# Performance work log

Hardware: AMD Instinct MI355X
Metric: run time of the kernel (lower is better)

Reference implementation:

```python
import jax, jax.numpy as jnp
import numpy as np

B, T, D = 1, 2048, 4096
H, G = 32, 8
HD = D // H          # 128
REP = H // G         # 4
KV_DIM = 2 * HD * G  # 2048


def setup_inputs() -> dict:
    key = jax.random.key(0)
    k0, k1, k2, k3 = jax.random.split(key, 4)
    x = jax.random.normal(k0, (B, T, D), dtype=jnp.float32)
    Wq = jax.random.normal(k1, (D, D), dtype=jnp.float32) * 0.02
    Wkv = jax.random.normal(k2, (D, KV_DIM), dtype=jnp.float32) * 0.02
    Wo = jax.random.normal(k3, (D, D), dtype=jnp.float32) * 0.02
    bo = jnp.zeros((D,), dtype=jnp.float32)
    return {"x": x, "Wq": Wq, "Wkv": Wkv, "Wo": Wo, "bo": bo}


def reference(x, Wq, Wkv, Wo, bo):
    b, t, d = x.shape
    # projections (qkv_bias=False)
    q = jnp.dot(x, Wq).reshape(b, t, H, HD).transpose(0, 2, 1, 3)        # (b,H,t,hd)
    kv = jnp.dot(x, Wkv).reshape(b, t, G, 2, HD).transpose(2, 3, 0, 1, 4)  # (G,2,b,t,hd)
    k, v = kv[:, 0], kv[:, 1]                                             # (G,b,t,hd)
    # faithful to torch: unsqueeze+repeat then flat view(b, H, t, hd)
    k = jnp.broadcast_to(k[:, :, None], (G, b, REP, t, HD)).reshape(b, H, t, HD)
    v = jnp.broadcast_to(v[:, :, None], (G, b, REP, t, HD)).reshape(b, H, t, HD)
    # attention: mask then scale, matching original order
    scores = jnp.einsum('bhqd,bhkd->bhqk', q, k)                          # (b,H,t,t)
    causal = jnp.triu(jnp.ones((t, t), dtype=bool), 1)
    scores = jnp.where(causal[None, None], -jnp.inf, scores)
    weights = jax.nn.softmax(scores * (1.0 / HD ** 0.5), axis=-1)
    ctx = jnp.einsum('bhqk,bhkd->bhqd', weights, v)                       # (b,H,t,hd)
    ctx = ctx.transpose(0, 2, 1, 3).reshape(b, t, d)
    return jnp.dot(ctx, Wo) + bo
```

## Files before the change

### kernel.cpp

```cpp
#include <hip/hip_runtime.h>

#define T_SEQ 2048
#define D_MODEL 4096
#define NH 32
#define NG 8
#define HD 128

typedef unsigned short u16;
typedef __bf16 bf16x8 __attribute__((ext_vector_type(8)));
typedef float f32x4 __attribute__((ext_vector_type(4)));

#define AS1 __attribute__((address_space(1)))
#define AS3 __attribute__((address_space(3)))

__device__ __forceinline__ void async_cp16(const u16* g, u16* l) {
  __builtin_amdgcn_global_load_lds((AS1 void*)g, (AS3 void*)l, 16, 0, 0);
}

__device__ __forceinline__ u16 f2bf(float f){
  union { float f; unsigned x; } v; v.f = f;
  unsigned r = v.x + 0x7FFFu + ((v.x >> 16) & 1u);
  return (u16)(r >> 16);
}
__device__ __forceinline__ u16 to_bf(float f){ return f2bf(f); }
__device__ __forceinline__ u16 to_bf(u16 u){ return u; }

__global__ __launch_bounds__(256) void cvt_k(const float* __restrict__ in,
                                             u16* __restrict__ out, int n4)
{
  int i = blockIdx.x * 256 + threadIdx.x;
  if (i >= n4) return;
  float4 v = *(const float4*)&in[(size_t)i * 4];
  short4 o;
  o.x = (short)f2bf(v.x); o.y = (short)f2bf(v.y);
  o.z = (short)f2bf(v.z); o.w = (short)f2bf(v.w);
  *(short4*)&out[(size_t)i * 4] = o;
}

template<typename TIN>
__global__ __launch_bounds__(256) void transpose_k(const TIN* __restrict__ in,
                                                   u16* __restrict__ out, int R, int C)
{
  int z = blockIdx.z;
  in  += (size_t)z * R * C;
  out += (size_t)z * R * C;
  __shared__ __align__(16) u16 tile[32][36];
  int c0 = blockIdx.x * 32, r0 = blockIdx.y * 32;
  int t = threadIdx.x;
  int lr = t >> 3, lc = (t & 7) * 4;
  const TIN* src = &in[(size_t)(r0 + lr) * C + c0 + lc];
  #pragma unroll
  for (int i = 0; i < 4; i++) tile[lr][lc + i] = to_bf(src[i]);
  __syncthreads();
  short4 v;
  v.x = (short)tile[lc + 0][lr];
  v.y = (short)tile[lc + 1][lr];
  v.z = (short)tile[lc + 2][lr];
  v.w = (short)tile[lc + 3][lr];
  *(short4*)&out[(size_t)(c0 + lr) * R + r0 + lc] = v;
}

template<int MODE>
__global__ __launch_bounds__(256) void gemm_k(
    const u16* __restrict__ A, const u16* __restrict__ BT,
    u16* __restrict__ Cout, u16* __restrict__ Kout, u16* __restrict__ Vout,
    float* __restrict__ Fout, const float* __restrict__ bias, int K, int N)
{
  __shared__ __align__(16) u16 sA[128 * 64];
  __shared__ __align__(16) u16 sB[128 * 64];
  const int t = threadIdx.x;
  const int lane = t & 63, wave = t >> 6;
  const int quad = lane >> 4, lm = lane & 15;
  const int wm = wave >> 1, wn = wave & 1;
  const int m0 = blockIdx.y * 128, n0 = blockIdx.x * 128;
  const f32x4 fzero = {0.f, 0.f, 0.f, 0.f};

  const int sr_sub = lane >> 3;
  const int sgl = (lane & 7) ^ sr_sub;

  f32x4 acc[4][4];
  #pragma unroll
  for (int i = 0; i < 4; i++)
    #pragma unroll
    for (int j = 0; j < 4; j++) acc[i][j] = fzero;

  for (int k0 = 0; k0 < K; k0 += 64) {
    #pragma unroll
    for (int c = 0; c < 4; c++) {
      int r = c * 32 + wave * 8 + sr_sub;
      async_cp16(&A [(size_t)(m0 + r) * K + k0 + sgl * 8], &sA[(c * 256 + wave * 64) * 8]);
      async_cp16(&BT[(size_t)(n0 + r) * K + k0 + sgl * 8], &sB[(c * 256 + wave * 64) * 8]);
    }
    __syncthreads();
    #pragma unroll
    for (int kb = 0; kb < 2; kb++) {
      bf16x8 af[4], bfr[4];
      #pragma unroll
      for (int mt = 0; mt < 4; mt++) {
        int row = wm * 64 + mt * 16 + lm;
        af[mt] = *(const bf16x8*)&sA[row * 64 + (((kb * 4 + quad) ^ (lm & 7)) * 8)];
      }
      #pragma unroll
      for (int nt = 0; nt < 4; nt++) {
        int row = wn * 64 + nt * 16 + lm;
        bfr[nt] = *(const bf16x8*)&sB[row * 64 + (((kb * 4 + quad) ^ (lm & 7)) * 8)];
      }
      #pragma unroll
      for (int mt = 0; mt < 4; mt++)
        #pragma unroll
        for (int nt = 0; nt < 4; nt++)
          acc[mt][nt] = __builtin_amdgcn_mfma_f32_16x16x32_bf16(af[mt], bfr[nt], acc[mt][nt], 0, 0, 0);
    }
    __syncthreads();
  }

  #pragma unroll
  for (int mt = 0; mt < 4; mt++) {
    #pragma unroll
    for (int nt = 0; nt < 4; nt++) {
      #pragma unroll
      for (int r = 0; r < 4; r++) {
        int grow = m0 + wm * 64 + mt * 16 + quad * 4 + r;
        int gcol = n0 + wn * 64 + nt * 16 + lm;
        float v = acc[mt][nt][r];
        if (MODE == 0) {
          Cout[(size_t)grow * N + gcol] = f2bf(v);
        } else if (MODE == 1) {
          int g = gcol >> 8, s = (gcol >> 7) & 1, hd = gcol & 127;
          u16* dst = s ? Vout : Kout;
          dst[((size_t)g * T_SEQ + grow) * HD + hd] = f2bf(v);
        } else {
          Fout[(size_t)grow * N + gcol] = v + bias[gcol];
        }
      }
    }
  }
}

__global__ __launch_bounds__(256) void attn_k(
    const u16* __restrict__ Q, const u16* __restrict__ Kb,
    const u16* __restrict__ Vt, u16* __restrict__ ctx)
{
  __shared__ __align__(16) u16 sK[2 * 64 * 128];
  __shared__ __align__(16) u16 sV[2 * 128 * 64];
  __shared__ __align__(16) u16 sP[4 * 16 * 72];
  const int t = threadIdx.x;
  const int lane = t & 63, wave = t >> 6;
  const int quad = lane >> 4, lm = lane & 15;

  const int id = blockIdx.x + gridDim.x * blockIdx.y;
  const int g = id & 7;
  const int idx = id >> 3;
  const int h = g * 4 + (idx & 3);
  const int q0 = (31 - (idx >> 2)) * 64;
  const int nt = (q0 >> 6) + 1;

  const float scale = 0.088388347648318447f;
  const float C1 = scale * 1.4426950408889634f;
  const float C2 = -14.0f * 1.4426950408889634f;
  const f32x4 fzero = {0.f, 0.f, 0.f, 0.f};

  bf16x8 aq[4];
  {
    const u16* qp = Q + (size_t)(q0 + wave * 16 + lm) * D_MODEL + h * HD + quad * 8;
    #pragma unroll
    for (int kb = 0; kb < 4; kb++) aq[kb] = *(const bf16x8*)(qp + kb * 32);
  }
  f32x4 o[8];
  #pragma unroll
  for (int i = 0; i < 8; i++) o[i] = fzero;
  float l4[4];
  #pragma unroll
  for (int r = 0; r < 4; r++) l4[r] = 0.f;

  const u16* Kg = Kb + (size_t)g * T_SEQ * HD;
  const u16* Vg = Vt + (size_t)g * HD * T_SEQ;
  u16* sPw = sP + wave * 16 * 72;

  const int k_r_sub = lane >> 4;
  const int v_r_sub = lane >> 3;
  const int v_gl = (lane & 7) ^ v_r_sub;

  auto stage = [&](int td) {
    const int kv0 = td << 6;
    u16* dK = sK + (td & 1) * (64 * 128);
    u16* dV = sV + (td & 1) * (128 * 64);
    #pragma unroll
    for (int c = 0; c < 4; c++) {
      int rk = c * 16 + wave * 4 + k_r_sub;
      int kgl = (lane & 15) ^ (rk & 7);
      async_cp16(&Kg[(size_t)(kv0 + rk) * HD + kgl * 8], &dK[(c * 256 + wave * 64) * 8]);
      int rv = c * 32 + wave * 8 + v_r_sub;
      async_cp16(&Vg[(size_t)rv * T_SEQ + kv0 + v_gl * 8], &dV[(c * 256 + wave * 64) * 8]);
    }
  };

  stage(0);
  if (nt > 1) stage(1);

  for (int ti = 0; ti < nt; ++ti) {
    if (ti + 1 < nt) { asm volatile("s_waitcnt vmcnt(8)" ::: "memory"); }
    else             { asm volatile("s_waitcnt vmcnt(0)" ::: "memory"); }
    __builtin_amdgcn_s_barrier();

    const u16* cK = sK + (ti & 1) * (64 * 128);
    const u16* cV = sV + (ti & 1) * (128 * 64);
    const int kv0 = ti << 6;

    f32x4 s[4];
    __builtin_amdgcn_s_setprio(1);
    #pragma unroll
    for (int nt4 = 0; nt4 < 4; nt4++) {
      s[nt4] = fzero;
      #pragma unroll
      for (int kb = 0; kb < 4; kb++) {
        int row = nt4 * 16 + lm;
        bf16x8 bk = *(const bf16x8*)&cK[row * 128 + (((kb * 4 + quad) ^ (lm & 7)) * 8)];
        s[nt4] = __builtin_amdgcn_mfma_f32_16x16x32_bf16(aq[kb], bk, s[nt4], 0, 0, 0);
      }
    }
    __builtin_amdgcn_s_setprio(0);

    #pragma unroll
    for (int r = 0; r < 4; r++) {
      int qr = q0 + wave * 16 + quad * 4 + r;
      #pragma unroll
      for (int nt4 = 0; nt4 < 4; nt4++) {
        int kvc = kv0 + nt4 * 16 + lm;
        float p = exp2f(fmaf(s[nt4][r], C1, C2));
        p = (kvc > qr) ? 0.f : p;
        l4[r] += p;
        sPw[(quad * 4 + r) * 72 + nt4 * 16 + lm] = f2bf(p);
      }
    }

    __builtin_amdgcn_s_setprio(1);
    #pragma unroll
    for (int kb2 = 0; kb2 < 2; kb2++) {
      bf16x8 ap = *(const bf16x8*)&sPw[lm * 72 + kb2 * 32 + quad * 8];
      #pragma unroll
      for (int n8 = 0; n8 < 8; n8++) {
        int row = n8 * 16 + lm;
        bf16x8 bv = *(const bf16x8*)&cV[row * 64 + (((kb2 * 4 + quad) ^ (lm & 7)) * 8)];
        o[n8] = __builtin_amdgcn_mfma_f32_16x16x32_bf16(ap, bv, o[n8], 0, 0, 0);
      }
    }
    __builtin_amdgcn_s_setprio(0);

    __builtin_amdgcn_s_barrier();
    if (ti + 2 < nt) stage(ti + 2);
  }

  #pragma unroll
  for (int r = 0; r < 4; r++) {
    #pragma unroll
    for (int off = 1; off < 16; off <<= 1) l4[r] += __shfl_xor(l4[r], off, 64);
  }

  #pragma unroll
  for (int r = 0; r < 4; r++) {
    float inv = 1.f / l4[r];
    #pragma unroll
    for (int n8 = 0; n8 < 8; n8++) {
      ctx[(size_t)(q0 + wave * 16 + quad * 4 + r) * D_MODEL + h * HD + n8 * 16 + lm]
          = f2bf(o[n8][r] * inv);
    }
  }
}

extern "C" void kernel_launch(void* const* d_in, const int* in_sizes, int n_in,
                              void* d_out, int out_size, void* d_ws, size_t ws_size,
                              hipStream_t stream)
{
  const float* x   = (const float*)d_in[0];
  const float* Wq  = (const float*)d_in[1];
  const float* Wkv = (const float*)d_in[2];
  const float* Wo  = (const float*)d_in[3];
  const float* bo  = (const float*)d_in[4];
  float* out = (float*)d_out;

  char* ws = (char*)d_ws;
  const size_t SZ_T   = 33554432;
  const size_t SZ_ACT = 16777216;
  const size_t SZ_KV  = 4194304;
  u16* Tb = (u16*)(ws);
  u16* Xb = (u16*)(ws + SZ_T);
  u16* Qb = (u16*)(ws + SZ_T + SZ_ACT);
  u16* Cx = (u16*)(ws + SZ_T + 2 * SZ_ACT);
  u16* Kb = (u16*)(ws + SZ_T + 3 * SZ_ACT);
  u16* Vb = (u16*)(ws + SZ_T + 3 * SZ_ACT + SZ_KV);
  u16* Vt = (u16*)(ws + SZ_T + 3 * SZ_ACT + 2 * SZ_KV);

  cvt_k<<<dim3(8192, 1, 1), 256, 0, stream>>>(x, Xb, 2097152);
  transpose_k<float><<<dim3(128, 128, 1), 256, 0, stream>>>(Wq, Tb, 4096, 4096);
  gemm_k<0><<<dim3(32, 16, 1), 256, 0, stream>>>(Xb, Tb, Qb, nullptr, nullptr, nullptr, nullptr, 4096, 4096);
  transpose_k<float><<<dim3(64, 128, 1), 256, 0, stream>>>(Wkv, Tb, 4096, 2048);
  gemm_k<1><<<dim3(16, 16, 1), 256, 0, stream>>>(Xb, Tb, nullptr, Kb, Vb, nullptr, nullptr, 4096, 2048);
  transpose_k<u16><<<dim3(4, 64, 8), 256, 0, stream>>>(Vb, Vt, 2048, 128);
  attn_k<<<dim3(32, 32, 1), 256, 0, stream>>>(Qb, Kb, Vt, Cx);
  transpose_k<float><<<dim3(128, 128, 1), 256, 0, stream>>>(Wo, Tb, 4096, 4096);
  gemm_k<2><<<dim3(32, 16, 1), 256, 0, stream>>>(Cx, Tb, nullptr, nullptr, nullptr, out, bo, 4096, 4096);
}
```

Measured before the change: 516.2 us.

## Double-buffer GEMM LDS tiles and write V transposed from KV GEMM epilogue

The GEMM kernel now double-buffers its A/B LDS tiles, prefetching two k-steps ahead with async global-to-LDS copies, partial vmcnt waits and raw barriers, mirroring the attention kernel's pipeline. The aim is to overlap global loads with MFMA work instead of serialising load then compute. The KV-projection epilogue also writes V directly in transposed layout with packed short4 stores, removing the separate V transpose kernel and its buffer. Doubling LDS use per block may reduce occupancy, and the transposed V stores are strided across rows.

```diff
diff --git a/kernel.cpp b/kernel.cpp
--- a/kernel.cpp
+++ b/kernel.cpp
@@ -66,13 +66,14 @@
     u16* __restrict__ Cout, u16* __restrict__ Kout, u16* __restrict__ Vout,
     float* __restrict__ Fout, const float* __restrict__ bias, int K, int N)
 {
-  __shared__ __align__(16) u16 sA[128 * 64];
-  __shared__ __align__(16) u16 sB[128 * 64];
+  __shared__ __align__(16) u16 sA[2 * 128 * 64];
+  __shared__ __align__(16) u16 sB[2 * 128 * 64];
   const int t = threadIdx.x;
   const int lane = t & 63, wave = t >> 6;
   const int quad = lane >> 4, lm = lane & 15;
   const int wm = wave >> 1, wn = wave & 1;
   const int m0 = blockIdx.y * 128, n0 = blockIdx.x * 128;
+  const int ntk = K >> 6;
   const f32x4 fzero = {0.f, 0.f, 0.f, 0.f};
 
   const int sr_sub = lane >> 3;
@@ -84,26 +85,43 @@
     #pragma unroll
     for (int j = 0; j < 4; j++) acc[i][j] = fzero;
 
-  for (int k0 = 0; k0 < K; k0 += 64) {
+  auto stage = [&](int td) {
+    const int k0 = td << 6;
+    u16* dA = sA + (td & 1) * (128 * 64);
+    u16* dB = sB + (td & 1) * (128 * 64);
     #pragma unroll
     for (int c = 0; c < 4; c++) {
       int r = c * 32 + wave * 8 + sr_sub;
-      async_cp16(&A [(size_t)(m0 + r) * K + k0 + sgl * 8], &sA[(c * 256 + wave * 64) * 8]);
-      async_cp16(&BT[(size_t)(n0 + r) * K + k0 + sgl * 8], &sB[(c * 256 + wave * 64) * 8]);
-    }
-    __syncthreads();
+      async_cp16(&A [(size_t)(m0 + r) * K + k0 + sgl * 8], &dA[(c * 256 + wave * 64) * 8]);
+      async_cp16(&BT[(size_t)(n0 + r) * K + k0 + sgl * 8], &dB[(c * 256 + wave * 64) * 8]);
+    }
+  };
+
+  stage(0);
+  stage(1);
+
+  for (int ti = 0; ti < ntk; ++ti) {
+    if (ti + 1 < ntk) { asm volatile("s_waitcnt vmcnt(8)" ::: "memory"); }
+    else             { asm volatile("s_waitcnt vmcnt(0)" ::: "memory"); }
+    __builtin_amdgcn_s_barrier();
+    asm volatile("" ::: "memory");
+
+    const u16* cA = sA + (ti & 1) * (128 * 64);
+    const u16* cB = sB + (ti & 1) * (128 * 64);
+
+    __builtin_amdgcn_s_setprio(1);
     #pragma unroll
     for (int kb = 0; kb < 2; kb++) {
       bf16x8 af[4], bfr[4];
       #pragma unroll
       for (int mt = 0; mt < 4; mt++) {
         int row = wm * 64 + mt * 16 + lm;
-        af[mt] = *(const bf16x8*)&sA[row * 64 + (((kb * 4 + quad) ^ (lm & 7)) * 8)];
+        af[mt] = *(const bf16x8*)&cA[row * 64 + (((kb * 4 + quad) ^ (lm & 7)) * 8)];
       }
       #pragma unroll
       for (int nt = 0; nt < 4; nt++) {
         int row = wn * 64 + nt * 16 + lm;
-        bfr[nt] = *(const bf16x8*)&sB[row * 64 + (((kb * 4 + quad) ^ (lm & 7)) * 8)];
+        bfr[nt] = *(const bf16x8*)&cB[row * 64 + (((kb * 4 + quad) ^ (lm & 7)) * 8)];
       }
       #pragma unroll
       for (int mt = 0; mt < 4; mt++)
@@ -111,26 +129,40 @@
         for (int nt = 0; nt < 4; nt++)
           acc[mt][nt] = __builtin_amdgcn_mfma_f32_16x16x32_bf16(af[mt], bfr[nt], acc[mt][nt], 0, 0, 0);
     }
-    __syncthreads();
+    __builtin_amdgcn_s_setprio(0);
+
+    __builtin_amdgcn_s_barrier();
+    asm volatile("" ::: "memory");
+    if (ti + 2 < ntk) stage(ti + 2);
   }
 
   #pragma unroll
   for (int mt = 0; mt < 4; mt++) {
     #pragma unroll
     for (int nt = 0; nt < 4; nt++) {
-      #pragma unroll
-      for (int r = 0; r < 4; r++) {
-        int grow = m0 + wm * 64 + mt * 16 + quad * 4 + r;
-        int gcol = n0 + wn * 64 + nt * 16 + lm;
-        float v = acc[mt][nt][r];
-        if (MODE == 0) {
-          Cout[(size_t)grow * N + gcol] = f2bf(v);
-        } else if (MODE == 1) {
-          int g = gcol >> 8, s = (gcol >> 7) & 1, hd = gcol & 127;
-          u16* dst = s ? Vout : Kout;
-          dst[((size_t)g * T_SEQ + grow) * HD + hd] = f2bf(v);
-        } else {
-          Fout[(size_t)grow * N + gcol] = v + bias[gcol];
+      int gcol = n0 + wn * 64 + nt * 16 + lm;
+      int grow0 = m0 + wm * 64 + mt * 16 + quad * 4;
+      if (MODE == 1 && ((gcol >> 7) & 1)) {
+        int g = gcol >> 8, hd = gcol & 127;
+        short4 pv;
+        pv.x = (short)f2bf(acc[mt][nt][0]);
+        pv.y = (short)f2bf(acc[mt][nt][1]);
+        pv.z = (short)f2bf(acc[mt][nt][2]);
+        pv.w = (short)f2bf(acc[mt][nt][3]);
+        *(short4*)&Vout[((size_t)g * HD + hd) * T_SEQ + grow0] = pv;
+      } else {
+        #pragma unroll
+        for (int r = 0; r < 4; r++) {
+          int grow = grow0 + r;
+          float v = acc[mt][nt][r];
+          if (MODE == 0) {
+            Cout[(size_t)grow * N + gcol] = f2bf(v);
+          } else if (MODE == 1) {
+            int g = gcol >> 8, hd = gcol & 127;
+            Kout[((size_t)g * T_SEQ + grow) * HD + hd] = f2bf(v);
+          } else {
+            Fout[(size_t)grow * N + gcol] = v + bias[gcol];
+          }
         }
       }
     }
@@ -202,6 +234,7 @@
     if (ti + 1 < nt) { asm volatile("s_waitcnt vmcnt(8)" ::: "memory"); }
     else             { asm volatile("s_waitcnt vmcnt(0)" ::: "memory"); }
     __builtin_amdgcn_s_barrier();
+    asm volatile("" ::: "memory");
 
     const u16* cK = sK + (ti & 1) * (64 * 128);
     const u16* cV = sV + (ti & 1) * (128 * 64);
@@ -248,6 +281,7 @@
     __builtin_amdgcn_s_setprio(0);
 
     __builtin_amdgcn_s_barrier();
+    asm volatile("" ::: "memory");
     if (ti + 2 < nt) stage(ti + 2);
   }
 
@@ -288,15 +322,13 @@
   u16* Qb = (u16*)(ws + SZ_T + SZ_ACT);
   u16* Cx = (u16*)(ws + SZ_T + 2 * SZ_ACT);
   u16* Kb = (u16*)(ws + SZ_T + 3 * SZ_ACT);
-  u16* Vb = (u16*)(ws + SZ_T + 3 * SZ_ACT + SZ_KV);
-  u16* Vt = (u16*)(ws + SZ_T + 3 * SZ_ACT + 2 * SZ_KV);
+  u16* Vt = (u16*)(ws + SZ_T + 3 * SZ_ACT + SZ_KV);
 
   cvt_k<<<dim3(8192, 1, 1), 256, 0, stream>>>(x, Xb, 2097152);
   transpose_k<float><<<dim3(128, 128, 1), 256, 0, stream>>>(Wq, Tb, 4096, 4096);
   gemm_k<0><<<dim3(32, 16, 1), 256, 0, stream>>>(Xb, Tb, Qb, nullptr, nullptr, nullptr, nullptr, 4096, 4096);
   transpose_k<float><<<dim3(64, 128, 1), 256, 0, stream>>>(Wkv, Tb, 4096, 2048);
-  gemm_k<1><<<dim3(16, 16, 1), 256, 0, stream>>>(Xb, Tb, nullptr, Kb, Vb, nullptr, nullptr, 4096, 2048);
-  transpose_k<u16><<<dim3(4, 64, 8), 256, 0, stream>>>(Vb, Vt, 2048, 128);
+  gemm_k<1><<<dim3(16, 16, 1), 256, 0, stream>>>(Xb, Tb, nullptr, Kb, Vt, nullptr, nullptr, 4096, 2048);
   attn_k<<<dim3(32, 32, 1), 256, 0, stream>>>(Qb, Kb, Vt, Cx);
   transpose_k<float><<<dim3(128, 128, 1), 256, 0, stream>>>(Wo, Tb, 4096, 4096);
   gemm_k<2><<<dim3(32, 16, 1), 256, 0, stream>>>(Cx, Tb, nullptr, nullptr, nullptr, out, bo, 4096, 4096);
```

New measurement: 488.8 us. 1.06x faster.
